# Optimization experiments

Measured on AMD Instinct MI355X. Metric: run time of the kernel, lower is better.

## Reference

```python
import jax, jax.numpy as jnp
import numpy as np

B, S, H, HS, BLK = 4, 4096, 16, 1024, 64
D = HS // H


def setup_inputs() -> dict:
    key = jax.random.key(0)
    ks = jax.random.split(key, 7)
    s = np.float32(1.0 / np.sqrt(HS))
    return {
        "hidden_states": jax.random.normal(ks[0], (B, S, HS), jnp.float32),
        "Wq": jax.random.normal(ks[1], (HS, HS), jnp.float32) * s,
        "bq": jax.random.normal(ks[2], (HS,), jnp.float32) * s,
        "Wk": jax.random.normal(ks[3], (HS, HS), jnp.float32) * s,
        "bk": jax.random.normal(ks[4], (HS,), jnp.float32) * s,
        "Wv": jax.random.normal(ks[5], (HS, HS), jnp.float32) * s,
        "bv": jax.random.normal(ks[6], (HS,), jnp.float32) * s,
    }


def reference(hidden_states, Wq, bq, Wk, bk, Wv, bv):
    b, m, _ = hidden_states.shape
    h, d, wm = H, D, BLK
    wn = wm
    nb = m // wm  # number of blocks
    scale = np.float32(1.0 / np.sqrt(d))

    def heads(x):  # [b, m, hs] -> [b, h, m, d]
        return x.reshape(b, m, h, d).transpose(0, 2, 1, 3)

    q = heads(hidden_states @ Wq.T + bq)
    k = heads(hidden_states @ Wk.T + bk)
    v = heads(hidden_states @ Wv.T + bv)

    qb = q.reshape(b, h, nb, wm, d)
    kb = k.reshape(b, h, nb, wn, d)
    vb = v.reshape(b, h, nb, wn, d)

    def attend(qx, kx, vx):  # qx [b,h,Q,d], kx/vx [b,h,K,d]
        scores = jnp.einsum('bhqd,bhkd->bhqk', qx, kx) * scale
        return jnp.einsum('bhqk,bhkd->bhqd', jax.nn.softmax(scores, axis=-1), vx)

    # first block: full attention over all keys
    first_ctx = attend(qb[:, :, 0], k, v)[:, :, None]

    # second block: keys = blocks [0, 1, 2, -1]
    k2 = jnp.concatenate([kb[:, :, 0], kb[:, :, 1], kb[:, :, 2], kb[:, :, -1]], axis=2)
    v2 = jnp.concatenate([vb[:, :, 0], vb[:, :, 1], vb[:, :, 2], vb[:, :, -1]], axis=2)
    second_ctx = attend(qb[:, :, 1], k2, v2)[:, :, None]

    # middle blocks 2..nb-3: sliding window of 3 key blocks + global first/last
    exp_k = jnp.concatenate([kb[:, :, 1:-3], kb[:, :, 2:-2], kb[:, :, 3:-1]], axis=3)  # [b,h,l,3wn,d]
    exp_v = jnp.concatenate([vb[:, :, 1:-3], vb[:, :, 2:-2], vb[:, :, 3:-1]], axis=3)
    mq = qb[:, :, 2:-2]  # [b,h,l,wm,d]
    inner = jnp.einsum('bhlqd,bhlkd->bhlqk', mq, exp_k) * scale
    first_band = jnp.einsum('bhlqd,bhkd->bhlqk', mq, kb[:, :, 0]) * scale
    last_band = jnp.einsum('bhlqd,bhkd->bhlqk', mq, kb[:, :, -1]) * scale
    band = jnp.concatenate([first_band, inner, last_band], axis=-1)  # [b,h,l,wm,5wn]
    aw = jax.nn.softmax(band, axis=-1)
    mid_ctx = jnp.einsum('bhlqk,bhlkd->bhlqd', aw[..., wn:4 * wn], exp_v)
    mid_ctx = mid_ctx + jnp.einsum('bhlqk,bhkd->bhlqd', aw[..., :wn], vb[:, :, 0])
    mid_ctx = mid_ctx + jnp.einsum('bhlqk,bhkd->bhlqd', aw[..., -wn:], vb[:, :, -1])

    # second-to-last block: keys = blocks [0, -3, -2, -1]
    k3 = jnp.concatenate([kb[:, :, 0], kb[:, :, -3], kb[:, :, -2], kb[:, :, -1]], axis=2)
    v3 = jnp.concatenate([vb[:, :, 0], vb[:, :, -3], vb[:, :, -2], vb[:, :, -1]], axis=2)
    second_last_ctx = attend(qb[:, :, -2], k3, v3)[:, :, None]

    # last block: full attention over all keys
    last_ctx = attend(qb[:, :, -1], k, v)[:, :, None]

    ctx = jnp.concatenate([first_ctx, second_ctx, mid_ctx, second_last_ctx, last_ctx], axis=2)
    return ctx.reshape(b, h, m, d).transpose(0, 2, 1, 3).reshape(b, m, h * d)
```

## Files before the change

### kernel.cpp

```cpp
#include <hip/hip_runtime.h>

typedef unsigned short u16;
using f32x4  = __attribute__((ext_vector_type(4))) float;
using bf16x8 = __attribute__((ext_vector_type(8))) short;

#define SEQ 4096
#define HS  1024
#define NHEAD 16
#define DH  64

__device__ __forceinline__ u16 f2bf(float f) {
  unsigned u = __float_as_uint(f);
  unsigned r = (u + 0x7fffu + ((u >> 16) & 1u)) >> 16;
  return (u16)r;
}

__device__ __forceinline__ void gl_lds16(const void* g, void* l) {
  __builtin_amdgcn_global_load_lds(
      (const __attribute__((address_space(1))) unsigned int*)g,
      (__attribute__((address_space(3))) unsigned int*)l, 16, 0, 0);
}

#define LGKM0 asm volatile("s_waitcnt lgkmcnt(0)" ::: "memory")
#define BARR  __builtin_amdgcn_s_barrier()

__global__ void cvt_kernel(const float* __restrict__ src, u16* __restrict__ dst, int n) {
  int idx = blockIdx.x * blockDim.x + threadIdx.x;
  int stride = gridDim.x * blockDim.x;
  for (int i = idx * 4; i < n; i += stride * 4) {
    float4 v = *reinterpret_cast<const float4*>(src + i);
    u16 o0 = f2bf(v.x), o1 = f2bf(v.y), o2 = f2bf(v.z), o3 = f2bf(v.w);
    unsigned lo = (unsigned)o0 | ((unsigned)o1 << 16);
    unsigned hi = (unsigned)o2 | ((unsigned)o3 << 16);
    uint2 pk; pk.x = lo; pk.y = hi;
    *reinterpret_cast<uint2*>(dst + i) = pk;
  }
}

__global__ void cvt_w_kernel(const float* __restrict__ w0, const float* __restrict__ w1,
                             const float* __restrict__ w2,
                             u16* __restrict__ d0, u16* __restrict__ d1, u16* __restrict__ d2,
                             int n) {
  const float* s; u16* d;
  if (blockIdx.y == 0) { s = w0; d = d0; }
  else if (blockIdx.y == 1) { s = w1; d = d1; }
  else { s = w2; d = d2; }
  int idx = blockIdx.x * blockDim.x + threadIdx.x;
  int stride = gridDim.x * blockDim.x;
  for (int i = idx * 4; i < n; i += stride * 4) {
    float4 v = *reinterpret_cast<const float4*>(s + i);
    u16 o0 = f2bf(v.x), o1 = f2bf(v.y), o2 = f2bf(v.z), o3 = f2bf(v.w);
    unsigned lo = (unsigned)o0 | ((unsigned)o1 << 16);
    unsigned hi = (unsigned)o2 | ((unsigned)o3 << 16);
    uint2 pk; pk.x = lo; pk.y = hi;
    *reinterpret_cast<uint2*>(d + i) = pk;
  }
}

__global__ __launch_bounds__(512) void gemm_qkv8(
    const u16* __restrict__ X,
    const u16* __restrict__ Wq, const u16* __restrict__ Wk, const u16* __restrict__ Wv,
    const float* __restrict__ bq, const float* __restrict__ bk, const float* __restrict__ bv,
    u16* __restrict__ Q, u16* __restrict__ K, u16* __restrict__ V) {
  const u16* W; const float* bias; u16* O;
  if (blockIdx.z == 0)      { W = Wq; bias = bq; O = Q; }
  else if (blockIdx.z == 1) { W = Wk; bias = bk; O = K; }
  else                      { W = Wv; bias = bv; O = V; }

  __shared__ u16 lds[65536];

  const int tid = threadIdx.x;
  const int l = tid & 63;
  const int w = tid >> 6;
  const int wr = w >> 2;
  const int wc = w & 3;
  const int c = l & 15;
  const int g = l >> 4;

  int flat = blockIdx.x;
  int swz = (flat & 7) * 32 + (flat >> 3);
  const int n0 = (swz >> 6) * 256;
  const int m0 = (swz & 63) * 256;

  f32x4 acc[2][4][4] = {};

  auto stage = [&](const u16* G, int gbase, int ktile, int kh, int which) {
    u16* region = lds + ((ktile & 1) * 32768 + which * 16384 + kh * 8192);
#pragma unroll
    for (int i = 0; i < 2; ++i) {
      int chunk = w * 2 + i;
      int srow = chunk * 8 + (l >> 3);
      int slot = (l & 7) ^ (l >> 3);
      int grow = srow + ((slot >> 2) << 7);
      int ke = ktile * 64 + kh * 32 + (slot & 3) * 8;
      gl_lds16(G + (size_t)(gbase + grow) * HS + ke, region + chunk * 512);
    }
  };

  auto readA = [&](int cur, int CH, int KH, bf16x8* aq) {
    const char* base = (const char*)lds + cur * 65536 + KH * 16384;
    int colb = (wr * 64 + g * 16) ^ ((c & 7) << 4);
#pragma unroll
    for (int mf = 0; mf < 4; ++mf)
      aq[mf] = *reinterpret_cast<const bf16x8*>(base + (CH * 64 + mf * 16 + c) * 128 + colb);
  };
  auto readB = [&](int cur, int KH, bf16x8* bq) {
    const char* base = (const char*)lds + cur * 65536 + 32768 + KH * 16384;
    int colb = ((wc >> 1) * 64 + g * 16) ^ ((c & 7) << 4);
#pragma unroll
    for (int nf = 0; nf < 4; ++nf)
      bq[nf] = *reinterpret_cast<const bf16x8*>(base + ((wc & 1) * 64 + nf * 16 + c) * 128 + colb);
  };
  auto mma16 = [&](bf16x8* aq, bf16x8* bq, f32x4 (*accr)[4]) {
    __builtin_amdgcn_s_setprio(1);
#pragma unroll
    for (int mf = 0; mf < 4; ++mf)
#pragma unroll
      for (int nf = 0; nf < 4; ++nf)
        accr[mf][nf] = __builtin_amdgcn_mfma_f32_16x16x32_bf16(aq[mf], bq[nf], accr[mf][nf], 0, 0, 0);
    __builtin_amdgcn_s_setprio(0);
  };

  stage(X, m0, 0, 0, 0); stage(W, n0, 0, 0, 1);
  stage(X, m0, 0, 1, 0); stage(W, n0, 0, 1, 1);
  stage(X, m0, 1, 0, 0); stage(W, n0, 1, 0, 1);
  asm volatile("s_waitcnt vmcnt(4)" ::: "memory");
  BARR;

  for (int j = 0; j < 16; ++j) {
    const int cur = j & 1;
    bf16x8 aq[4], bq[4];
    readA(cur, 0, 0, aq); readB(cur, 0, bq);
    if (j + 1 < 16) stage(X, m0, j + 1, 1, 0);
    BARR; LGKM0; mma16(aq, bq, acc[0]); BARR;
    readA(cur, 1, 0, aq);
    if (j + 1 < 16) stage(W, n0, j + 1, 1, 1);
    BARR; LGKM0; mma16(aq, bq, acc[1]); BARR;
    readA(cur, 0, 1, aq); readB(cur, 1, bq);
    if (j + 2 < 16) stage(X, m0, j + 2, 0, 0);
    BARR; LGKM0; mma16(aq, bq, acc[0]); BARR;
    readA(cur, 1, 1, aq);
    if (j + 2 < 16) stage(W, n0, j + 2, 0, 1);
    BARR; LGKM0; mma16(aq, bq, acc[1]);
    if (j < 14)       asm volatile("s_waitcnt vmcnt(4)" ::: "memory");
    else if (j == 14) asm volatile("s_waitcnt vmcnt(0)" ::: "memory");
    BARR;
  }

#pragma unroll
  for (int nf = 0; nf < 4; ++nf) {
    int cc = n0 + wc * 64 + nf * 16 + c;
    float bval = bias[cc];
#pragma unroll
    for (int ch = 0; ch < 2; ++ch)
#pragma unroll
      for (int mf = 0; mf < 4; ++mf)
#pragma unroll
        for (int jj = 0; jj < 4; ++jj) {
          int r = m0 + wr * 128 + ch * 64 + mf * 16 + g * 4 + jj;
          O[(size_t)r * HS + cc] = f2bf(acc[ch][mf][nf][jj] + bval);
        }
  }
}

__global__ void bigbird_attn2(const u16* __restrict__ Q, const u16* __restrict__ K,
                              const u16* __restrict__ V, float* __restrict__ OUT,
                              float* __restrict__ Opart, float* __restrict__ MLpart) {
  __shared__ u16 Qs[64 * 64];
  __shared__ u16 Ks[2][64 * 64];
  __shared__ u16 Vt[64 * 72];
  __shared__ u16 Ps[64 * 72];

  const int tid = threadIdx.x;
  const int lane = tid & 63;
  const int w = tid >> 6;
  const int g = lane >> 4;
  const int c = lane & 15;

  int bid = blockIdx.x;
  int qb, b, h, nkb, seg4 = 0, p = 0;
  bool heavy;
  if (bid < 3968) {
    heavy = false;
    b = bid & 3; int t = bid >> 2; h = t & 15; qb = (t >> 4) + 1;
    nkb = (qb == 1 || qb == 62) ? 4 : 5;
  } else {
    heavy = true;
    int t = bid - 3968;
    b = t & 3; t >>= 2; h = t & 15; t >>= 4;
    int seg = t & 15; int q2 = t >> 4;
    qb = q2 ? 63 : 0; seg4 = seg * 4; nkb = 4;
    p = ((q2 * 16 + h) * 4 + b) * 16 + seg;
  }

  const size_t base_bh = (size_t)b * SEQ * HS + (size_t)h * DH;

  auto kb_of = [&](int it) -> int {
    if (heavy) return seg4 + it;
    if (qb == 1)  return (it == 3) ? 63 : it;
    if (qb == 62) return (it == 0) ? 0 : 60 + it;
    return (it == 0) ? 0 : ((it == 4) ? 63 : qb - 2 + it);
  };

  {
    const u16* qg = Q + base_bh + (size_t)qb * 64 * HS;
#pragma unroll
    for (int t2 = 0; t2 < 2; ++t2) {
      int sub = w * 2 + t2;
      int r = sub * 8 + (lane >> 3);
      int c16 = (lane & 7) ^ (r & 7);
      gl_lds16(qg + (size_t)r * HS + c16 * 8, Qs + sub * 512);
    }
  }
  int kb0 = kb_of(0);
  {
    const u16* kg = K + base_bh + (size_t)kb0 * 64 * HS;
#pragma unroll
    for (int t2 = 0; t2 < 2; ++t2) {
      int sub = w * 2 + t2;
      int r = sub * 8 + (lane >> 3);
      int c16 = (lane & 7) ^ (r & 7);
      gl_lds16(kg + (size_t)r * HS + c16 * 8, Ks[0] + sub * 512);
    }
  }
  bf16x8 vr0, vr1;
  {
    const u16* vg = V + base_bh + (size_t)kb0 * 64 * HS;
    int krow = tid >> 2, dseg = (tid & 3) * 16;
    vr0 = *reinterpret_cast<const bf16x8*>(vg + (size_t)krow * HS + dseg);
    vr1 = *reinterpret_cast<const bf16x8*>(vg + (size_t)krow * HS + dseg + 8);
  }
  __syncthreads();

  bf16x8 qf[2];
#pragma unroll
  for (int ks = 0; ks < 2; ++ks) {
    int r = w * 16 + c;
    int c16 = (ks * 4 + g) ^ (r & 7);
    qf[ks] = *reinterpret_cast<const bf16x8*>(Qs + r * 64 + c16 * 8);
  }

  float m_run = -1e30f, l_run = 0.f;
  f32x4 o_acc[4] = {};
  const float scale = 0.125f;

  for (int it = 0; it < nkb; ++it) {
    const int cur = it & 1;
    {
      int krow = tid >> 2, dseg = (tid & 3) * 16;
#pragma unroll
      for (int j2 = 0; j2 < 8; ++j2) {
        Vt[(dseg + j2) * 72 + krow]     = (u16)vr0[j2];
        Vt[(dseg + 8 + j2) * 72 + krow] = (u16)vr1[j2];
      }
    }
    if (it + 1 < nkb) {
      int kbn = kb_of(it + 1);
      const u16* kg = K + base_bh + (size_t)kbn * 64 * HS;
#pragma unroll
      for (int t2 = 0; t2 < 2; ++t2) {
        int sub = w * 2 + t2;
        int r = sub * 8 + (lane >> 3);
        int c16 = (lane & 7) ^ (r & 7);
        gl_lds16(kg + (size_t)r * HS + c16 * 8, Ks[cur ^ 1] + sub * 512);
      }
      const u16* vg = V + base_bh + (size_t)kbn * 64 * HS;
      int krow = tid >> 2, dseg = (tid & 3) * 16;
      vr0 = *reinterpret_cast<const bf16x8*>(vg + (size_t)krow * HS + dseg);
      vr1 = *reinterpret_cast<const bf16x8*>(vg + (size_t)krow * HS + dseg + 8);
    }

    f32x4 accs[4] = {};
#pragma unroll
    for (int ks = 0; ks < 2; ++ks) {
#pragma unroll
      for (int mf = 0; mf < 4; ++mf) {
        int r = mf * 16 + c;
        int c16 = (ks * 4 + g) ^ (r & 7);
        bf16x8 kf = *reinterpret_cast<const bf16x8*>(Ks[cur] + r * 64 + c16 * 8);
        accs[mf] = __builtin_amdgcn_mfma_f32_16x16x32_bf16(kf, qf[ks], accs[mf], 0, 0, 0);
      }
    }

    float sv[16];
    float smax = -1e30f;
#pragma unroll
    for (int mf = 0; mf < 4; ++mf)
#pragma unroll
      for (int j = 0; j < 4; ++j) {
        float s = accs[mf][j] * scale;
        sv[mf * 4 + j] = s;
        smax = fmaxf(smax, s);
      }
    smax = fmaxf(smax, __shfl_xor(smax, 16));
    smax = fmaxf(smax, __shfl_xor(smax, 32));
    float m_new = fmaxf(m_run, smax);
    float corr = __expf(m_run - m_new);
    float psum = 0.f;
    u16 pb[16];
#pragma unroll
    for (int i = 0; i < 16; ++i) {
      float pv = __expf(sv[i] - m_new);
      psum += pv;
      pb[i] = f2bf(pv);
    }
    psum += __shfl_xor(psum, 16);
    psum += __shfl_xor(psum, 32);
    l_run = l_run * corr + psum;
    m_run = m_new;

#pragma unroll
    for (int j = 0; j < 4; ++j) {
      float cj = __shfl(corr, g * 4 + j);
#pragma unroll
      for (int df = 0; df < 4; ++df) o_acc[df][j] *= cj;
    }

    {
      int r = w * 16 + c;
#pragma unroll
      for (int mf = 0; mf < 4; ++mf) {
        unsigned lo = (unsigned)pb[mf * 4 + 0] | ((unsigned)pb[mf * 4 + 1] << 16);
        unsigned hi = (unsigned)pb[mf * 4 + 2] | ((unsigned)pb[mf * 4 + 3] << 16);
        uint2 pk; pk.x = lo; pk.y = hi;
        *reinterpret_cast<uint2*>(Ps + r * 72 + mf * 16 + g * 4) = pk;
      }
    }

    __syncthreads();

#pragma unroll
    for (int ks = 0; ks < 2; ++ks) {
      bf16x8 pf = *reinterpret_cast<const bf16x8*>(Ps + (w * 16 + c) * 72 + ks * 32 + g * 8);
#pragma unroll
      for (int df = 0; df < 4; ++df) {
        bf16x8 vf = *reinterpret_cast<const bf16x8*>(Vt + (df * 16 + c) * 72 + ks * 32 + g * 8);
        o_acc[df] = __builtin_amdgcn_mfma_f32_16x16x32_bf16(pf, vf, o_acc[df], 0, 0, 0);
      }
    }

    __syncthreads();
  }

  if (!heavy) {
#pragma unroll
    for (int j = 0; j < 4; ++j) {
      float lr = __shfl(l_run, g * 4 + j);
      float inv = 1.f / lr;
      int r = qb * 64 + w * 16 + g * 4 + j;
      size_t rowbase = ((size_t)b * SEQ + r) * HS + (size_t)h * DH;
#pragma unroll
      for (int df = 0; df < 4; ++df)
        OUT[rowbase + df * 16 + c] = o_acc[df][j] * inv;
    }
  } else {
#pragma unroll
    for (int j = 0; j < 4; ++j) {
      int row = w * 16 + g * 4 + j;
#pragma unroll
      for (int df = 0; df < 4; ++df)
        Opart[(size_t)p * 4096 + row * 64 + df * 16 + c] = o_acc[df][j];
    }
    if (g == 0) {
      int row = w * 16 + c;
      MLpart[(size_t)p * 128 + row * 2]     = m_run;
      MLpart[(size_t)p * 128 + row * 2 + 1] = l_run;
    }
  }
}

__global__ void bigbird_combine(const float* __restrict__ Opart, const float* __restrict__ MLpart,
                                float* __restrict__ OUT) {
  int bid = blockIdx.x;
  int b = bid & 3; int t = bid >> 2; int h = t & 15; int q2 = t >> 4;
  int qb = q2 ? 63 : 0;
  int w = threadIdx.x >> 6, lane = threadIdx.x & 63;
  int pbase = ((q2 * 16 + h) * 4 + b) * 16;
#pragma unroll 1
  for (int rr = 0; rr < 16; ++rr) {
    int row = w * 16 + rr;
    float ms[16], ls[16];
    float M = -1e30f;
#pragma unroll
    for (int s = 0; s < 16; ++s) {
      ms[s] = MLpart[(size_t)(pbase + s) * 128 + row * 2];
      ls[s] = MLpart[(size_t)(pbase + s) * 128 + row * 2 + 1];
      M = fmaxf(M, ms[s]);
    }
    float L = 0.f, acc = 0.f;
#pragma unroll
    for (int s = 0; s < 16; ++s) {
      float e = __expf(ms[s] - M);
      L += ls[s] * e;
      acc += e * Opart[(size_t)(pbase + s) * 4096 + row * 64 + lane];
    }
    int r = qb * 64 + row;
    OUT[((size_t)b * SEQ + r) * HS + (size_t)h * DH + lane] = acc / L;
  }
}

extern "C" void kernel_launch(void* const* d_in, const int* in_sizes, int n_in,
                              void* d_out, int out_size, void* d_ws, size_t ws_size,
                              hipStream_t stream) {
  const float* X  = (const float*)d_in[0];
  const float* Wq = (const float*)d_in[1];
  const float* bq = (const float*)d_in[2];
  const float* Wk = (const float*)d_in[3];
  const float* bk = (const float*)d_in[4];
  const float* Wv = (const float*)d_in[5];
  const float* bv = (const float*)d_in[6];
  float* out = (float*)d_out;

  u16* Xb  = (u16*)d_ws;
  u16* Wqb = Xb + 16777216;
  u16* Wkb = Wqb + 1048576;
  u16* Wvb = Wkb + 1048576;
  u16* Qb  = Wvb + 1048576;
  u16* Kb  = Qb + 16777216;
  u16* Vb  = Kb + 16777216;

  float* Opart  = (float*)Xb;
  float* MLpart = (float*)Wqb;

  cvt_kernel<<<2048, 256, 0, stream>>>(X, Xb, 16777216);
  cvt_w_kernel<<<dim3(256, 3), 256, 0, stream>>>(Wq, Wk, Wv, Wqb, Wkb, Wvb, 1048576);
  gemm_qkv8<<<dim3(256, 1, 3), 512, 0, stream>>>(Xb, Wqb, Wkb, Wvb, bq, bk, bv, Qb, Kb, Vb);
  bigbird_attn2<<<6016, 256, 0, stream>>>(Qb, Kb, Vb, out, Opart, MLpart);
  bigbird_combine<<<128, 256, 0, stream>>>(Opart, MLpart, out);
}
```

Before: 259.9 us.

## Stage QKV GEMM epilogue through LDS for coalesced stores and remap tiles

The QKV projection GEMM now writes its bf16 output tile into shared memory first, then issues 16-byte row-contiguous global stores, replacing the scattered 2-byte stores per accumulator element. The launch grid is also flattened to 768 blocks with a new block-to-tile mapping that groups tiles sharing the same X rows across Q/K/V and column tiles, which should improve L2 reuse. The cost is extra LDS traffic, added barriers in the epilogue, and a padded 260-element row stride that may cause some bank conflicts.

```diff
diff --git a/kernel.cpp b/kernel.cpp
--- a/kernel.cpp
+++ b/kernel.cpp
@@ -62,11 +62,6 @@
     const u16* __restrict__ Wq, const u16* __restrict__ Wk, const u16* __restrict__ Wv,
     const float* __restrict__ bq, const float* __restrict__ bk, const float* __restrict__ bv,
     u16* __restrict__ Q, u16* __restrict__ K, u16* __restrict__ V) {
-  const u16* W; const float* bias; u16* O;
-  if (blockIdx.z == 0)      { W = Wq; bias = bq; O = Q; }
-  else if (blockIdx.z == 1) { W = Wk; bias = bk; O = K; }
-  else                      { W = Wv; bias = bv; O = V; }
-
   __shared__ u16 lds[65536];
 
   const int tid = threadIdx.x;
@@ -77,18 +72,25 @@
   const int c = l & 15;
   const int g = l >> 4;
 
-  int flat = blockIdx.x;
-  int swz = (flat & 7) * 32 + (flat >> 3);
-  const int n0 = (swz >> 6) * 256;
-  const int m0 = (swz & 63) * 256;
+  int i = blockIdx.x;
+  int k8 = i & 7, j8 = i >> 3;
+  int w2 = j8 >> 5, r8 = j8 & 31;
+  int np = w2 * 4 + (r8 >> 3);
+  int mp = k8 * 8 + (r8 & 7);
+  const int m0 = mp * 256;
+  const int mat = np >> 2;
+  const int n0 = (np & 3) * 256;
+  const u16* W = (mat == 0) ? Wq : (mat == 1) ? Wk : Wv;
+  const float* bias = (mat == 0) ? bq : (mat == 1) ? bk : bv;
+  u16* O = (mat == 0) ? Q : (mat == 1) ? K : V;
 
   f32x4 acc[2][4][4] = {};
 
   auto stage = [&](const u16* G, int gbase, int ktile, int kh, int which) {
     u16* region = lds + ((ktile & 1) * 32768 + which * 16384 + kh * 8192);
 #pragma unroll
-    for (int i = 0; i < 2; ++i) {
-      int chunk = w * 2 + i;
+    for (int ii = 0; ii < 2; ++ii) {
+      int chunk = w * 2 + ii;
       int srow = chunk * 8 + (l >> 3);
       int slot = (l & 7) ^ (l >> 3);
       int grow = srow + ((slot >> 2) << 7);
@@ -104,20 +106,20 @@
     for (int mf = 0; mf < 4; ++mf)
       aq[mf] = *reinterpret_cast<const bf16x8*>(base + (CH * 64 + mf * 16 + c) * 128 + colb);
   };
-  auto readB = [&](int cur, int KH, bf16x8* bq) {
+  auto readB = [&](int cur, int KH, bf16x8* bq2) {
     const char* base = (const char*)lds + cur * 65536 + 32768 + KH * 16384;
     int colb = ((wc >> 1) * 64 + g * 16) ^ ((c & 7) << 4);
 #pragma unroll
     for (int nf = 0; nf < 4; ++nf)
-      bq[nf] = *reinterpret_cast<const bf16x8*>(base + ((wc & 1) * 64 + nf * 16 + c) * 128 + colb);
+      bq2[nf] = *reinterpret_cast<const bf16x8*>(base + ((wc & 1) * 64 + nf * 16 + c) * 128 + colb);
   };
-  auto mma16 = [&](bf16x8* aq, bf16x8* bq, f32x4 (*accr)[4]) {
+  auto mma16 = [&](bf16x8* aq, bf16x8* bq2, f32x4 (*accr)[4]) {
     __builtin_amdgcn_s_setprio(1);
 #pragma unroll
     for (int mf = 0; mf < 4; ++mf)
 #pragma unroll
       for (int nf = 0; nf < 4; ++nf)
-        accr[mf][nf] = __builtin_amdgcn_mfma_f32_16x16x32_bf16(aq[mf], bq[nf], accr[mf][nf], 0, 0, 0);
+        accr[mf][nf] = __builtin_amdgcn_mfma_f32_16x16x32_bf16(aq[mf], bq2[nf], accr[mf][nf], 0, 0, 0);
     __builtin_amdgcn_s_setprio(0);
   };
 
@@ -129,37 +131,55 @@
 
   for (int j = 0; j < 16; ++j) {
     const int cur = j & 1;
-    bf16x8 aq[4], bq[4];
-    readA(cur, 0, 0, aq); readB(cur, 0, bq);
+    bf16x8 aq[4], bq2[4];
+    readA(cur, 0, 0, aq); readB(cur, 0, bq2);
     if (j + 1 < 16) stage(X, m0, j + 1, 1, 0);
-    BARR; LGKM0; mma16(aq, bq, acc[0]); BARR;
+    BARR; LGKM0; mma16(aq, bq2, acc[0]); BARR;
     readA(cur, 1, 0, aq);
     if (j + 1 < 16) stage(W, n0, j + 1, 1, 1);
-    BARR; LGKM0; mma16(aq, bq, acc[1]); BARR;
-    readA(cur, 0, 1, aq); readB(cur, 1, bq);
+    BARR; LGKM0; mma16(aq, bq2, acc[1]); BARR;
+    readA(cur, 0, 1, aq); readB(cur, 1, bq2);
     if (j + 2 < 16) stage(X, m0, j + 2, 0, 0);
-    BARR; LGKM0; mma16(aq, bq, acc[0]); BARR;
+    BARR; LGKM0; mma16(aq, bq2, acc[0]); BARR;
     readA(cur, 1, 1, aq);
     if (j + 2 < 16) stage(W, n0, j + 2, 0, 1);
-    BARR; LGKM0; mma16(aq, bq, acc[1]);
+    BARR; LGKM0; mma16(aq, bq2, acc[1]);
     if (j < 14)       asm volatile("s_waitcnt vmcnt(4)" ::: "memory");
     else if (j == 14) asm volatile("s_waitcnt vmcnt(0)" ::: "memory");
     BARR;
   }
 
-#pragma unroll
-  for (int nf = 0; nf < 4; ++nf) {
-    int cc = n0 + wc * 64 + nf * 16 + c;
-    float bval = bias[cc];
-#pragma unroll
-    for (int ch = 0; ch < 2; ++ch)
-#pragma unroll
-      for (int mf = 0; mf < 4; ++mf)
-#pragma unroll
-        for (int jj = 0; jj < 4; ++jj) {
-          int r = m0 + wr * 128 + ch * 64 + mf * 16 + g * 4 + jj;
-          O[(size_t)r * HS + cc] = f2bf(acc[ch][mf][nf][jj] + bval);
+  __syncthreads();
+  {
+    u16* cst = lds;
+#pragma unroll 1
+    for (int p = 0; p < 2; ++p) {
+      if (wr == p) {
+#pragma unroll
+        for (int nf = 0; nf < 4; ++nf) {
+          int cc = wc * 64 + nf * 16 + c;
+          float bval = bias[n0 + cc];
+#pragma unroll
+          for (int ch = 0; ch < 2; ++ch)
+#pragma unroll
+            for (int mf = 0; mf < 4; ++mf)
+#pragma unroll
+              for (int jj = 0; jj < 4; ++jj) {
+                int rl = ch * 64 + mf * 16 + g * 4 + jj;
+                cst[rl * 260 + cc] = f2bf(acc[ch][mf][nf][jj] + bval);
+              }
         }
+      }
+      __syncthreads();
+#pragma unroll
+      for (int i2 = 0; i2 < 8; ++i2) {
+        int row = i2 * 16 + (tid >> 5);
+        int colu = (tid & 31) * 8;
+        bf16x8 vv = *reinterpret_cast<const bf16x8*>(cst + row * 260 + colu);
+        *reinterpret_cast<bf16x8*>(O + (size_t)(m0 + p * 128 + row) * HS + n0 + colu) = vv;
+      }
+      __syncthreads();
+    }
   }
 }
 
@@ -424,7 +444,7 @@
 
   cvt_kernel<<<2048, 256, 0, stream>>>(X, Xb, 16777216);
   cvt_w_kernel<<<dim3(256, 3), 256, 0, stream>>>(Wq, Wk, Wv, Wqb, Wkb, Wvb, 1048576);
-  gemm_qkv8<<<dim3(256, 1, 3), 512, 0, stream>>>(Xb, Wqb, Wkb, Wvb, bq, bk, bv, Qb, Kb, Vb);
+  gemm_qkv8<<<768, 512, 0, stream>>>(Xb, Wqb, Wkb, Wvb, bq, bk, bv, Qb, Kb, Vb);
   bigbird_attn2<<<6016, 256, 0, stream>>>(Qb, Kb, Vb, out, Opart, MLpart);
   bigbird_combine<<<128, 256, 0, stream>>>(Opart, MLpart, out);
 }
```

Result: faster. 245.8 us (-5.4%).
